# Kernel tuning notes

Measured on AMD Instinct MI355X. Metric: run time of the kernel, lower is better.

## Reference

```python
import jax, jax.numpy as jnp
import numpy as np

B, N = 512, 4
OBS, OBSU, ID = 128, 64, 16
STATE = OBS + OBSU - ID  # 176
M1, M2, G1, A = 256, 256, 256, 16
E = 128  # hypernet_embed


def setup_inputs() -> dict:
    key = jax.random.key(0)
    ks = jax.random.split(key, 24)

    def W(k, shape):
        return jax.random.normal(k, shape, dtype=jnp.float32) * 0.05

    inp = {"input": jax.random.normal(ks[0], (B, N, OBS + OBSU), dtype=jnp.float32)}
    # layer1_hypernet: Linear(ID, 10*E)
    inp["l1_W"] = W(ks[1], (10 * E, ID)); inp["l1_b"] = W(ks[2], (10 * E,))
    # hyper_net{i}_w / hyper_net{i}_b : Linear(E, in*out) / Linear(E, out)
    inp["w1W"] = W(ks[3], (STATE * M1, E)); inp["w1b"] = W(ks[4], (STATE * M1,))
    inp["b1W"] = W(ks[5], (M1, E));        inp["b1b"] = W(ks[6], (M1,))
    inp["w2W"] = W(ks[7], (M1 * M2, E));   inp["w2b"] = W(ks[8], (M1 * M2,))
    inp["b2W"] = W(ks[9], (M2, E));        inp["b2b"] = W(ks[10], (M2,))
    inp["w3W"] = W(ks[11], (M2 * M2, E));  inp["w3b"] = W(ks[12], (M2 * M2,))
    inp["b3W"] = W(ks[13], (M2, E));       inp["b3b"] = W(ks[14], (M2,))
    inp["w4W"] = W(ks[15], (M2 * G1, E));  inp["w4b"] = W(ks[16], (M2 * G1,))
    inp["b4W"] = W(ks[17], (G1, E));       inp["b4b"] = W(ks[18], (G1,))
    inp["w5W"] = W(ks[19], (G1 * A, E));   inp["w5b"] = W(ks[20], (G1 * A,))
    inp["b5W"] = W(ks[21], (A, E));        inp["b5b"] = W(ks[22], (A,))
    return inp


def reference(input, l1_W, l1_b, w1W, w1b, b1W, b1b, w2W, w2b, b2W, b2b,
              w3W, w3b, b3W, b3b, w4W, w4b, b4W, b4b, w5W, w5b, b5W, b5b):
    b, n, d = input.shape
    BN = b * n
    ids = input[..., -ID:].reshape(BN, ID)
    x = input[..., :-ID].reshape(BN, d - ID)  # [BN, STATE]
    # layer1_hypernet: ReLU(Linear(ID -> 10E))
    h = jax.nn.relu(ids @ l1_W.T + l1_b)  # [BN, 10E]
    chunk = lambda i: h[:, i * E:(i + 1) * E]

    def layer(x, iw, ib, wW, wb, bW, bb, out_dim, act):
        # generate per-sample weight [BN, in, out] and bias [BN, out]
        Wm = (chunk(iw) @ wW.T + wb).reshape(BN, x.shape[-1], out_dim)
        bm = chunk(ib) @ bW.T + bb
        y = jnp.einsum('bs,bsm->bm', x, Wm) + bm  # batched GEMV
        return jax.nn.relu(y) if act else y

    out = layer(x,   0, 1, w1W, w1b, b1W, b1b, M1, True)
    out = layer(out, 2, 3, w2W, w2b, b2W, b2b, M2, True)
    out = layer(out, 4, 5, w3W, w3b, b3W, b3b, M2, True)
    out = layer(out, 6, 7, w4W, w4b, b4W, b4b, G1, False)  # no ReLU after layer 4
    out = layer(out, 8, 9, w5W, w5b, b5W, b5b, A, True)
    return out.reshape(b, n, A)
```

## Files before the change

### kernel.cpp

```cpp
#include <hip/hip_runtime.h>
#include <hip/hip_bf16.h>

#define E_ 128
#define NSAMP 2048

typedef __attribute__((ext_vector_type(8))) short short8;
typedef __attribute__((ext_vector_type(4))) float floatx4;

__device__ __forceinline__ ushort f2b(float f) {
    union { __hip_bfloat16 h; ushort u; } cv;
    cv.h = __float2bfloat16(f);
    return cv.u;
}

__device__ __forceinline__ void gload_lds16(const ushort* g, ushort* l) {
    __builtin_amdgcn_global_load_lds(
        (const __attribute__((address_space(1))) void*)g,
        (__attribute__((address_space(3))) void*)l, 16, 0, 0);
}

__global__ void hyper_h(const float* __restrict__ input, const float* __restrict__ l1W,
                        const float* __restrict__ l1b, float* __restrict__ h)
{
    int b = blockIdx.x / 5;
    int o = (blockIdx.x % 5) * 256 + threadIdx.x;
    const float* ids = input + (size_t)b * 192 + 176;
    const float* w = l1W + (size_t)o * 16;
    float a = l1b[o];
#pragma unroll
    for (int i = 0; i < 16; i += 4) {
        float4 wv = *(const float4*)(w + i);
        a += ids[i] * wv.x + ids[i + 1] * wv.y + ids[i + 2] * wv.z + ids[i + 3] * wv.w;
    }
    h[(size_t)b * 1280 + o] = fmaxf(a, 0.f);
}

__global__ void x0_t(const float* __restrict__ input, float* __restrict__ xT0)
{
    int idx = blockIdx.x * 256 + threadIdx.x;
    int s = idx >> 11, b = idx & 2047;
    xT0[idx] = input[(size_t)b * 192 + s];
}

__global__ void cvt_layer(const float* __restrict__ wW, const float* __restrict__ wb,
                          const float* __restrict__ bW, ushort* __restrict__ dst,
                          int S, int M)
{
    int i = (blockIdx.x * 256 + threadIdx.x) * 8;
    const int nW = S * M * E_;
    union { ushort o[8]; uint4 v; } u;
    if (i < nW) {
        float4 a = *(const float4*)(wW + i);
        float4 b = *(const float4*)(wW + i + 4);
        u.o[0] = f2b(a.x); u.o[1] = f2b(a.y); u.o[2] = f2b(a.z); u.o[3] = f2b(a.w);
        u.o[4] = f2b(b.x); u.o[5] = f2b(b.y); u.o[6] = f2b(b.z); u.o[7] = f2b(b.w);
    } else {
        int rem = i - nW;
        int slice = rem / (M * E_);
        int r2 = rem - slice * (M * E_);
        int m = r2 >> 7, e = r2 & 127;
        if (slice == 0) {
            const float* src = bW + (size_t)m * E_ + e;
            float4 a = *(const float4*)(src);
            float4 b = *(const float4*)(src + 4);
            u.o[0] = f2b(a.x); u.o[1] = f2b(a.y); u.o[2] = f2b(a.z); u.o[3] = f2b(a.w);
            u.o[4] = f2b(b.x); u.o[5] = f2b(b.y); u.o[6] = f2b(b.z); u.o[7] = f2b(b.w);
        } else {
#pragma unroll
            for (int jj = 0; jj < 8; ++jj) {
                int s = (slice - 1) * 128 + e + jj;
                u.o[jj] = (s < S) ? f2b(wb[(size_t)s * M + m]) : (ushort)0;
            }
        }
    }
    *(uint4*)(dst + i) = u.v;
}

struct P5 { const float* wW[5]; const float* wb[5]; const float* bW[5]; };

__global__ void prep(P5 p, ushort* __restrict__ dst,
                     const float* __restrict__ input, const float* __restrict__ l1W,
                     const float* __restrict__ l1b, float* __restrict__ h,
                     float* __restrict__ xT0)
{
    const int blk = blockIdx.x;
    if (blk < 15555) {
        const size_t offE[6] = {0, 5865472, 14352384, 22839296, 31326208, 31856640};
        const int Sl[5] = {176, 256, 256, 256, 256};
        const int Ml[5] = {256, 256, 256, 256, 16};
        size_t i = ((size_t)blk * 256 + threadIdx.x) * 8;
        if (i >= 31856640) return;
        int l = 0;
#pragma unroll
        for (int k = 1; k < 5; ++k) if (i >= offE[k]) l = k;
        const int S = Sl[l], M = Ml[l];
        const float* wW = p.wW[l];
        const float* wb = p.wb[l];
        const float* bW = p.bW[l];
        int r = (int)(i - offE[l]);
        const int nW = S * M * E_;
        union { ushort o[8]; uint4 v; } u;
        if (r < nW) {
            float4 a = *(const float4*)(wW + r);
            float4 b = *(const float4*)(wW + r + 4);
            u.o[0] = f2b(a.x); u.o[1] = f2b(a.y); u.o[2] = f2b(a.z); u.o[3] = f2b(a.w);
            u.o[4] = f2b(b.x); u.o[5] = f2b(b.y); u.o[6] = f2b(b.z); u.o[7] = f2b(b.w);
        } else {
            int rem = r - nW;
            int slice = rem / (M * E_);
            int r2 = rem - slice * (M * E_);
            int m = r2 >> 7, e = r2 & 127;
            if (slice == 0) {
                const float* src = bW + (size_t)m * E_ + e;
                float4 a = *(const float4*)(src);
                float4 b = *(const float4*)(src + 4);
                u.o[0] = f2b(a.x); u.o[1] = f2b(a.y); u.o[2] = f2b(a.z); u.o[3] = f2b(a.w);
                u.o[4] = f2b(b.x); u.o[5] = f2b(b.y); u.o[6] = f2b(b.z); u.o[7] = f2b(b.w);
            } else {
#pragma unroll
                for (int jj = 0; jj < 8; ++jj) {
                    int s = (slice - 1) * 128 + e + jj;
                    u.o[jj] = (s < S) ? f2b(wb[(size_t)s * M + m]) : (ushort)0;
                }
            }
        }
        *(uint4*)(dst + i) = u.v;
    } else if (blk < 15555 + 10240) {
        const int b2 = blk - 15555;
        const int b = b2 / 5;
        const int o = (b2 % 5) * 256 + threadIdx.x;
        const float* ids = input + (size_t)b * 192 + 176;
        const float* w = l1W + (size_t)o * 16;
        float a = l1b[o];
#pragma unroll
        for (int i = 0; i < 16; i += 4) {
            float4 wv = *(const float4*)(w + i);
            a += ids[i] * wv.x + ids[i + 1] * wv.y + ids[i + 2] * wv.z + ids[i + 3] * wv.w;
        }
        h[(size_t)b * 1280 + o] = fmaxf(a, 0.f);
    } else {
        const int idx = (blk - 25795) * 256 + threadIdx.x;
        const int s = idx >> 11, b = idx & 2047;
        xT0[idx] = input[(size_t)b * 192 + s];
    }
}

__global__ __launch_bounds__(256, 2) void gemm_big(
    const ushort* __restrict__ wWb, const float* __restrict__ h,
    const float* __restrict__ xT, float* __restrict__ partial,
    int S, int iw, int ksplit, int btiles, int ntiles)
{
    __shared__ __align__(16) ushort Bs[2][2 * 128 * 64];
    __shared__ __align__(16) float xs[17 * 128];

    const int tid = threadIdx.x;
    const int bid = blockIdx.x;
    const int xcd = bid & 7;
    const int jj_ = bid >> 3;
    const int combo = xcd + 8 * (jj_ / btiles);
    const int bt = jj_ % btiles;
    const int nt = combo % ntiles;
    const int ks = combo / ntiles;
    const int b0 = bt * 128;
    const int m0 = nt * 128;
    const int total_s = S + 3;
    const int base = total_s / ksplit;
    const int rem = total_s - base * ksplit;
    const int s0 = ks * base + min(ks, rem);
    const int s1v = s0 + base + (ks < rem ? 1 : 0);
    const int sE = min(s1v, S);
    const int ns = sE - s0;

    const int lane = tid & 63;
    const int wave = tid >> 6;
    const int quad = lane >> 4;
    const int lr = lane & 15;
    const int wm0 = wave * 32;

    const int brow = lane >> 3;
    const int bgg = (lane & 7) ^ brow;

    float hreg[2][2][2][8];
#pragma unroll
    for (int i = 0; i < 2; ++i)
#pragma unroll
        for (int p = 0; p < 2; ++p)
#pragma unroll
            for (int k2 = 0; k2 < 2; ++k2) {
                const float* src = h + (size_t)(b0 + wm0 + i * 16 + lr) * 1280
                                     + (size_t)iw * E_ + p * 64 + k2 * 32 + quad * 8;
                float4 v0 = *(const float4*)(src);
                float4 v1 = *(const float4*)(src + 4);
                hreg[i][p][k2][0] = v0.x; hreg[i][p][k2][1] = v0.y;
                hreg[i][p][k2][2] = v0.z; hreg[i][p][k2][3] = v0.w;
                hreg[i][p][k2][4] = v1.x; hreg[i][p][k2][5] = v1.y;
                hreg[i][p][k2][6] = v1.z; hreg[i][p][k2][7] = v1.w;
            }

    for (int idx = tid; idx < ns * 128; idx += 256) {
        int j = idx >> 7, bb2 = idx & 127;
        xs[idx] = xT[(size_t)(s0 + j) * NSAMP + b0 + bb2];
    }

    floatx4 acc[2][8];
#pragma unroll
    for (int i = 0; i < 2; ++i)
#pragma unroll
        for (int j = 0; j < 8; ++j)
            acc[i][j] = (floatx4){0.f, 0.f, 0.f, 0.f};

    auto dmaB = [&](int s, ushort* buf) {
#pragma unroll
        for (int p = 0; p < 2; ++p)
#pragma unroll
            for (int t4 = 0; t4 < 4; ++t4) {
                int rloc = wave * 32 + t4 * 8;
                const ushort* gp = wWb + ((size_t)s * 256 + m0 + rloc + brow) * E_ + p * 64 + bgg * 8;
                gload_lds16(gp, buf + (size_t)p * 8192 + (size_t)rloc * 64 + lane * 8);
            }
    };
    auto dmaBh = [&](int s, int p, ushort* buf) {
#pragma unroll
        for (int t4 = 0; t4 < 4; ++t4) {
            int rloc = wave * 32 + t4 * 8;
            const ushort* gp = wWb + ((size_t)s * 256 + m0 + rloc + brow) * E_ + p * 64 + bgg * 8;
            gload_lds16(gp, buf + (size_t)rloc * 64 + lane * 8);
        }
    };

    __builtin_amdgcn_sched_barrier(0);
    __syncthreads();
    __builtin_amdgcn_sched_barrier(0);
    dmaB(s0, &Bs[0][0]);
    if (ns > 1) dmaB(s0 + 1, &Bs[1][0]);

    for (int si = 0; si < ns; ++si) {
        const float xr0 = xs[si * 128 + wm0 + lr];
        const float xr1 = xs[si * 128 + wm0 + 16 + lr];
        short8 af0[2][2], af1[2][2];
#pragma unroll
        for (int p = 0; p < 2; ++p)
#pragma unroll
            for (int k2 = 0; k2 < 2; ++k2)
#pragma unroll
                for (int j = 0; j < 8; ++j) {
                    af0[p][k2][j] = (short)f2b(xr0 * hreg[0][p][k2][j]);
                    af1[p][k2][j] = (short)f2b(xr1 * hreg[1][p][k2][j]);
                }

        if (si + 1 < ns) asm volatile("s_waitcnt vmcnt(8)" ::: "memory");
        else             asm volatile("s_waitcnt vmcnt(0)" ::: "memory");
        __builtin_amdgcn_sched_barrier(0);
        __builtin_amdgcn_s_barrier();
        __builtin_amdgcn_sched_barrier(0);

        const ushort* bcur = &Bs[si & 1][0];
        __builtin_amdgcn_s_setprio(1);
#pragma unroll
        for (int kk = 0; kk < 4; ++kk) {
            const int p = kk >> 1, k2 = kk & 1;
            const int swz = ((k2 * 4 + quad) ^ (lr & 7)) * 8;
            short8 bfr[8];
#pragma unroll
            for (int j = 0; j < 8; ++j)
                bfr[j] = *(const short8*)&bcur[(size_t)p * 8192 + (size_t)(j * 16 + lr) * 64 + swz];
            const short8 a0 = (p == 0) ? ((k2 == 0) ? af0[0][0] : af0[0][1])
                                       : ((k2 == 0) ? af0[1][0] : af0[1][1]);
            const short8 a1 = (p == 0) ? ((k2 == 0) ? af1[0][0] : af1[0][1])
                                       : ((k2 == 0) ? af1[1][0] : af1[1][1]);
#pragma unroll
            for (int j = 0; j < 8; ++j) {
                acc[0][j] = __builtin_amdgcn_mfma_f32_16x16x32_bf16(a0, bfr[j], acc[0][j], 0, 0, 0);
                acc[1][j] = __builtin_amdgcn_mfma_f32_16x16x32_bf16(a1, bfr[j], acc[1][j], 0, 0, 0);
            }
        }
        __builtin_amdgcn_s_setprio(0);
        __builtin_amdgcn_sched_barrier(0);
        __builtin_amdgcn_s_barrier();
        __builtin_amdgcn_sched_barrier(0);

        if (si + 2 < ns) dmaB(s0 + si + 2, &Bs[si & 1][0]);
    }

    for (int s = sE; s < s1v; ++s) {
        for (int p = 0; p < 2; ++p) {
            __syncthreads();
            dmaBh(s, p, &Bs[0][0]);
            short8 af[2][2];
            if (s == S) {
#pragma unroll
                for (int k2 = 0; k2 < 2; ++k2)
#pragma unroll
                    for (int i = 0; i < 2; ++i) {
                        const float* src = h + (size_t)(b0 + wm0 + i * 16 + lr) * 1280
                                             + (size_t)(iw + 1) * E_ + p * 64 + k2 * 32 + quad * 8;
                        float4 v0 = *(const float4*)(src);
                        float4 v1 = *(const float4*)(src + 4);
                        af[k2][i][0] = (short)f2b(v0.x); af[k2][i][1] = (short)f2b(v0.y);
                        af[k2][i][2] = (short)f2b(v0.z); af[k2][i][3] = (short)f2b(v0.w);
                        af[k2][i][4] = (short)f2b(v1.x); af[k2][i][5] = (short)f2b(v1.y);
                        af[k2][i][6] = (short)f2b(v1.z); af[k2][i][7] = (short)f2b(v1.w);
                    }
            } else {
                const int jbase = (s - S - 1) * 128 + p * 64;
#pragma unroll
                for (int k2 = 0; k2 < 2; ++k2)
#pragma unroll
                    for (int i = 0; i < 2; ++i) {
                        const int b = b0 + wm0 + i * 16 + lr;
#pragma unroll
                        for (int jj = 0; jj < 8; ++jj) {
                            const int sp = jbase + k2 * 32 + quad * 8 + jj;
                            af[k2][i][jj] = (sp < S) ? (short)f2b(xT[(size_t)sp * NSAMP + b]) : (short)0;
                        }
                    }
            }
            __syncthreads();
#pragma unroll
            for (int k2 = 0; k2 < 2; ++k2) {
                const int swz = ((k2 * 4 + quad) ^ (lr & 7)) * 8;
                short8 bfr[8];
#pragma unroll
                for (int j = 0; j < 8; ++j)
                    bfr[j] = *(const short8*)&Bs[0][(size_t)(j * 16 + lr) * 64 + swz];
#pragma unroll
                for (int j = 0; j < 8; ++j) {
                    acc[0][j] = __builtin_amdgcn_mfma_f32_16x16x32_bf16(af[k2][0], bfr[j], acc[0][j], 0, 0, 0);
                    acc[1][j] = __builtin_amdgcn_mfma_f32_16x16x32_bf16(af[k2][1], bfr[j], acc[1][j], 0, 0, 0);
                }
            }
        }
    }

    float* dst = partial + (size_t)ks * NSAMP * 256;
#pragma unroll
    for (int i = 0; i < 2; ++i)
#pragma unroll
        for (int j = 0; j < 8; ++j)
#pragma unroll
            for (int r = 0; r < 4; ++r) {
                const int row = wm0 + i * 16 + quad * 4 + r;
                const int col = j * 16 + lr;
                dst[(size_t)(b0 + row) * 256 + m0 + col] = acc[i][j][r];
            }
}

template<int BM, int BN, int WROWS, int WCOLS>
__global__ __launch_bounds__(256, 2) void gemm_k(
    const ushort* __restrict__ wWb, const float* __restrict__ h,
    const float* __restrict__ xT, float* __restrict__ partial,
    int S, int M, int iw, int ksplit, int btiles, int ntiles)
{
    constexpr int SM = BM / WROWS / 16;
    constexpr int SN = BN / WCOLS / 16;
    constexpr int ASLOTS = BM * 8 / 256;
    constexpr int LDA = 72;

    __shared__ ushort As[BM][LDA];
    __shared__ ushort Bs[BN][LDA];

    const int tid = threadIdx.x;
    const int bt = blockIdx.x % btiles;
    const int nt = (blockIdx.x / btiles) % ntiles;
    const int ks = blockIdx.x / (btiles * ntiles);
    const int b0 = bt * BM;
    const int m0 = nt * BN;
    const int total_s = S + 3;
    const int base = total_s / ksplit;
    const int rem = total_s - base * ksplit;
    const int s0 = ks * base + min(ks, rem);
    const int s1 = s0 + base + (ks < rem ? 1 : 0);

    const int lane = tid & 63;
    const int wave = tid >> 6;
    const int quad = lane >> 4;
    const int lr = lane & 15;
    const int wm0 = (wave / WCOLS) * (BM / WROWS);
    const int wn0 = (wave % WCOLS) * (BN / WCOLS);

    const int tb = tid >> 3;
    const int teg = tid & 7;

    float hreg[ASLOTS][2][8];
#pragma unroll
    for (int k2 = 0; k2 < ASLOTS; ++k2) {
        int b = tb + 32 * k2;
#pragma unroll
        for (int p = 0; p < 2; ++p) {
            const float* src = h + (size_t)(b0 + b) * 1280 + (size_t)iw * E_ + p * 64 + teg * 8;
            float4 v0 = *(const float4*)(src);
            float4 v1 = *(const float4*)(src + 4);
            hreg[k2][p][0] = v0.x; hreg[k2][p][1] = v0.y; hreg[k2][p][2] = v0.z; hreg[k2][p][3] = v0.w;
            hreg[k2][p][4] = v1.x; hreg[k2][p][5] = v1.y; hreg[k2][p][6] = v1.z; hreg[k2][p][7] = v1.w;
        }
    }

    floatx4 acc[SM][SN];
#pragma unroll
    for (int i = 0; i < SM; ++i)
#pragma unroll
        for (int j = 0; j < SN; ++j)
            acc[i][j] = (floatx4){0.f, 0.f, 0.f, 0.f};

    for (int s = s0; s < s1; ++s) {
        float xv[ASLOTS];
        if (s < S) {
#pragma unroll
            for (int k2 = 0; k2 < ASLOTS; ++k2)
                xv[k2] = xT[(size_t)s * NSAMP + b0 + tb + 32 * k2];
        }

#pragma unroll
        for (int p = 0; p < 2; ++p) {
            if (s < S) {
#pragma unroll
                for (int k2 = 0; k2 < ASLOTS; ++k2) {
                    union { ushort o[8]; uint4 v; } u;
#pragma unroll
                    for (int j = 0; j < 8; ++j) u.o[j] = f2b(xv[k2] * hreg[k2][p][j]);
                    *(uint4*)&As[tb + 32 * k2][teg * 8] = u.v;
                }
            } else if (s == S) {
#pragma unroll
                for (int k2 = 0; k2 < ASLOTS; ++k2) {
                    const float* src = h + (size_t)(b0 + tb + 32 * k2) * 1280
                                         + (size_t)(iw + 1) * E_ + p * 64 + teg * 8;
                    float4 v0 = *(const float4*)(src);
                    float4 v1 = *(const float4*)(src + 4);
                    union { ushort o[8]; uint4 v; } u;
                    u.o[0] = f2b(v0.x); u.o[1] = f2b(v0.y); u.o[2] = f2b(v0.z); u.o[3] = f2b(v0.w);
                    u.o[4] = f2b(v1.x); u.o[5] = f2b(v1.y); u.o[6] = f2b(v1.z); u.o[7] = f2b(v1.w);
                    *(uint4*)&As[tb + 32 * k2][teg * 8] = u.v;
                }
            } else {
                int j0 = (s - S - 1) * 128 + p * 64 + teg * 8;
#pragma unroll
                for (int k2 = 0; k2 < ASLOTS; ++k2) {
                    int b = b0 + tb + 32 * k2;
                    union { ushort o[8]; uint4 v; } u;
#pragma unroll
                    for (int jj = 0; jj < 8; ++jj) {
                        int sp = j0 + jj;
                        u.o[jj] = (sp < S) ? f2b(xT[(size_t)sp * NSAMP + b]) : (ushort)0;
                    }
                    *(uint4*)&As[tb + 32 * k2][teg * 8] = u.v;
                }
            }
#pragma unroll
            for (int slot = tid; slot < BN * 8; slot += 256) {
                int m = slot >> 3, eg2 = slot & 7;
                *(uint4*)&Bs[m][eg2 * 8] =
                    *(const uint4*)(wWb + ((size_t)s * M + m0 + m) * E_ + p * 64 + eg2 * 8);
            }
            __syncthreads();
#pragma unroll
            for (int kk = 0; kk < 2; ++kk) {
                short8 af[SM], bfr[SN];
#pragma unroll
                for (int i = 0; i < SM; ++i)
                    af[i] = *(const short8*)&As[wm0 + i * 16 + lr][kk * 32 + quad * 8];
#pragma unroll
                for (int j = 0; j < SN; ++j)
                    bfr[j] = *(const short8*)&Bs[wn0 + j * 16 + lr][kk * 32 + quad * 8];
#pragma unroll
                for (int i = 0; i < SM; ++i)
#pragma unroll
                    for (int j = 0; j < SN; ++j)
                        acc[i][j] = __builtin_amdgcn_mfma_f32_16x16x32_bf16(af[i], bfr[j], acc[i][j], 0, 0, 0);
            }
            __syncthreads();
        }
    }

    float* dst = partial + (size_t)ks * NSAMP * M;
#pragma unroll
    for (int i = 0; i < SM; ++i)
#pragma unroll
        for (int j = 0; j < SN; ++j)
#pragma unroll
            for (int r = 0; r < 4; ++r) {
                int row = wm0 + i * 16 + quad * 4 + r;
                int col = wn0 + j * 16 + lr;
                dst[(size_t)(b0 + row) * M + m0 + col] = acc[i][j][r];
            }
}

__global__ void reduce_mid(const float* __restrict__ partial, const float* __restrict__ bb,
                           float* __restrict__ xTn, int KS, int relu)
{
    __shared__ float t[32][33];
    const int b0 = (blockIdx.x >> 3) * 32;
    const int m0 = (blockIdx.x & 7) * 32;
    const int mo = threadIdx.x & 31;
    const int bs0 = threadIdx.x >> 5;
    const float bv = bb[m0 + mo];
#pragma unroll
    for (int r = 0; r < 4; ++r) {
        const int bs = bs0 + 8 * r;
        const size_t off = (size_t)(b0 + bs) * 256 + m0 + mo;
        float a0 = 0.f, a1 = 0.f, a2 = 0.f, a3 = 0.f;
#pragma unroll
        for (int k = 0; k < 16; k += 4) {
            a0 += partial[(size_t)(k + 0) * (NSAMP * 256) + off];
            a1 += partial[(size_t)(k + 1) * (NSAMP * 256) + off];
            a2 += partial[(size_t)(k + 2) * (NSAMP * 256) + off];
            a3 += partial[(size_t)(k + 3) * (NSAMP * 256) + off];
        }
        float a = (a0 + a1) + (a2 + a3) + bv;
        if (relu) a = fmaxf(a, 0.f);
        t[bs][mo] = a;
    }
    __syncthreads();
    const int bo = threadIdx.x & 31;
    const int ms0 = threadIdx.x >> 5;
#pragma unroll
    for (int r = 0; r < 4; ++r) {
        const int ms = ms0 + 8 * r;
        xTn[(size_t)(m0 + ms) * NSAMP + b0 + bo] = t[bo][ms];
    }
}

__global__ void reduce_out(const float* __restrict__ partial, const float* __restrict__ bb,
                           float* __restrict__ out, int KS)
{
    int idx = blockIdx.x * 256 + threadIdx.x;
    float a0 = 0.f, a1 = 0.f, a2 = 0.f, a3 = 0.f;
#pragma unroll
    for (int k = 0; k < 64; k += 4) {
        a0 += partial[(size_t)(k + 0) * (NSAMP * 16) + idx];
        a1 += partial[(size_t)(k + 1) * (NSAMP * 16) + idx];
        a2 += partial[(size_t)(k + 2) * (NSAMP * 16) + idx];
        a3 += partial[(size_t)(k + 3) * (NSAMP * 16) + idx];
    }
    out[idx] = fmaxf((a0 + a1) + (a2 + a3) + bb[idx & 15], 0.f);
}

extern "C" void kernel_launch(void* const* d_in, const int* in_sizes, int n_in,
                              void* d_out, int out_size, void* d_ws, size_t ws_size,
                              hipStream_t stream)
{
    const float* input = (const float*)d_in[0];
    const float* l1W   = (const float*)d_in[1];
    const float* l1b   = (const float*)d_in[2];

    char* ws = (char*)d_ws;
    const int S_[5] = {176, 256, 256, 256, 256};
    const int M_[5] = {256, 256, 256, 256, 16};
    const size_t offE[6] = {0, 5865472, 14352384, 22839296, 31326208, 31856640};

    const bool fused = ws_size >= (size_t)111947776;

    ushort* wWb5;
    float *h, *xT0, *xT1, *part;
    if (fused) {
        wWb5 = (ushort*)(ws + 0);
        h    = (float*)(ws + 63713280);
        xT0  = (float*)(ws + 74199040);
        xT1  = (float*)(ws + 76296192);
        part = (float*)(ws + 78393344);
    } else {
        wWb5 = (ushort*)(ws + 0);
        h    = (float*)(ws + 16975872);
        xT0  = (float*)(ws + 27461632);
        xT1  = (float*)(ws + 29558784);
        part = (float*)(ws + 31655936);
    }

    if (fused) {
        P5 p;
        for (int i = 0; i < 5; ++i) {
            p.wW[i] = (const float*)d_in[3 + 4 * i];
            p.wb[i] = (const float*)d_in[4 + 4 * i];
            p.bW[i] = (const float*)d_in[5 + 4 * i];
        }
        hipLaunchKernelGGL(prep, dim3(27203), dim3(256), 0, stream,
                           p, wWb5, input, l1W, l1b, h, xT0);
    } else {
        hipLaunchKernelGGL(hyper_h, dim3(2048 * 5), dim3(256), 0, stream, input, l1W, l1b, h);
        hipLaunchKernelGGL(x0_t, dim3(176 * 2048 / 256), dim3(256), 0, stream, input, xT0);
    }

    float* xt[2] = {xT0, xT1};

    for (int i = 0; i < 5; ++i) {
        const float* wW = (const float*)d_in[3 + 4 * i];
        const float* wb = (const float*)d_in[4 + 4 * i];
        const float* bW = (const float*)d_in[5 + 4 * i];
        const float* bb = (const float*)d_in[6 + 4 * i];
        float* xin = xt[i & 1];

        ushort* wWbL;
        if (fused) {
            wWbL = wWb5 + offE[i];
        } else {
            wWbL = wWb5;
            int ntot = (S_[i] + 3) * M_[i] * E_;
            hipLaunchKernelGGL(cvt_layer, dim3(ntot / 2048), dim3(256), 0, stream,
                               wW, wb, bW, wWbL, S_[i], M_[i]);
        }

        if (M_[i] == 256) {
            const int btiles = 16, ntiles = 2, ksplit = 16;
            hipLaunchKernelGGL(gemm_big, dim3(btiles * ntiles * ksplit), dim3(256), 0, stream,
                               wWbL, h, xin, part, S_[i], 2 * i, ksplit, btiles, ntiles);
            hipLaunchKernelGGL(reduce_mid, dim3(512), dim3(256), 0, stream,
                               part, bb, xt[(i + 1) & 1], ksplit, (i < 3) ? 1 : 0);
        } else {
            const int btiles = 8, ntiles = 1, ksplit = 64;
            hipLaunchKernelGGL((gemm_k<256, 16, 4, 1>), dim3(btiles * ntiles * ksplit), dim3(256), 0, stream,
                               wWbL, h, xin, part, S_[i], 16, 2 * i, ksplit, btiles, ntiles);
            hipLaunchKernelGGL(reduce_out, dim3(128), dim3(256), 0, stream,
                               part, bb, (float*)d_out, ksplit);
        }
    }
}
```

Baseline: 500.2 us.

## Fuse split-K partial reduction and bias-ReLU into next layer's GEMM operand load

```diff
diff --git a/kernel.cpp b/kernel.cpp
--- a/kernel.cpp
+++ b/kernel.cpp
@@ -145,9 +145,11 @@
     }
 }
 
+template<int FUSED>
 __global__ __launch_bounds__(256, 2) void gemm_big(
     const ushort* __restrict__ wWb, const float* __restrict__ h,
-    const float* __restrict__ xT, float* __restrict__ partial,
+    const float* __restrict__ xsrc, const float* __restrict__ bbp,
+    float* __restrict__ partial,
     int S, int iw, int ksplit, int btiles, int ntiles)
 {
     __shared__ __align__(16) ushort Bs[2][2 * 128 * 64];
@@ -197,9 +199,34 @@
                 hreg[i][p][k2][6] = v1.z; hreg[i][p][k2][7] = v1.w;
             }
 
-    for (int idx = tid; idx < ns * 128; idx += 256) {
-        int j = idx >> 7, bb2 = idx & 127;
-        xs[idx] = xT[(size_t)(s0 + j) * NSAMP + b0 + bb2];
+    if constexpr (FUSED) {
+        const int sc = tid & 15;
+        const int br = tid >> 4;
+        for (int j0 = 0; j0 < ns; j0 += 16) {
+            const int j = j0 + sc;
+            if (j < ns) {
+                const float bv = bbp[s0 + j];
+#pragma unroll
+                for (int c = 0; c < 8; ++c) {
+                    const int b2 = c * 16 + br;
+                    const float* rp = xsrc + (size_t)(b0 + b2) * 256 + (s0 + j);
+                    float a0 = bv, a1 = 0.f, a2 = 0.f, a3 = 0.f;
+#pragma unroll
+                    for (int k = 0; k < 16; k += 4) {
+                        a0 += rp[(size_t)(k + 0) * (NSAMP * 256)];
+                        a1 += rp[(size_t)(k + 1) * (NSAMP * 256)];
+                        a2 += rp[(size_t)(k + 2) * (NSAMP * 256)];
+                        a3 += rp[(size_t)(k + 3) * (NSAMP * 256)];
+                    }
+                    xs[j * 128 + b2] = fmaxf((a0 + a1) + (a2 + a3), 0.f);
+                }
+            }
+        }
+    } else {
+        for (int idx = tid; idx < ns * 128; idx += 256) {
+            int j = idx >> 7, bb2 = idx & 127;
+            xs[idx] = xsrc[(size_t)(s0 + j) * NSAMP + b0 + bb2];
+        }
     }
 
     floatx4 acc[2][8];
@@ -301,6 +328,38 @@
                         af[k2][i][4] = (short)f2b(v1.x); af[k2][i][5] = (short)f2b(v1.y);
                         af[k2][i][6] = (short)f2b(v1.z); af[k2][i][7] = (short)f2b(v1.w);
                     }
+            } else if constexpr (FUSED) {
+                const int jbase = (s - S - 1) * 128 + p * 64;
+#pragma unroll
+                for (int k2 = 0; k2 < 2; ++k2)
+#pragma unroll
+                    for (int i = 0; i < 2; ++i) {
+                        const int b = b0 + wm0 + i * 16 + lr;
+                        const int spb = jbase + k2 * 32 + quad * 8;
+                        if (spb < S) {
+                            const float* rp = xsrc + (size_t)b * 256 + spb;
+                            float4 A0 = *(const float4*)(bbp + spb);
+                            float4 A1 = *(const float4*)(bbp + spb + 4);
+#pragma unroll 4
+                            for (int k = 0; k < 16; ++k) {
+                                float4 v0 = *(const float4*)(rp + (size_t)k * (NSAMP * 256));
+                                float4 v1 = *(const float4*)(rp + (size_t)k * (NSAMP * 256) + 4);
+                                A0.x += v0.x; A0.y += v0.y; A0.z += v0.z; A0.w += v0.w;
+                                A1.x += v1.x; A1.y += v1.y; A1.z += v1.z; A1.w += v1.w;
+                            }
+                            af[k2][i][0] = (short)f2b(fmaxf(A0.x, 0.f));
+                            af[k2][i][1] = (short)f2b(fmaxf(A0.y, 0.f));
+                            af[k2][i][2] = (short)f2b(fmaxf(A0.z, 0.f));
+                            af[k2][i][3] = (short)f2b(fmaxf(A0.w, 0.f));
+                            af[k2][i][4] = (short)f2b(fmaxf(A1.x, 0.f));
+                            af[k2][i][5] = (short)f2b(fmaxf(A1.y, 0.f));
+                            af[k2][i][6] = (short)f2b(fmaxf(A1.z, 0.f));
+                            af[k2][i][7] = (short)f2b(fmaxf(A1.w, 0.f));
+                        } else {
+#pragma unroll
+                            for (int jj = 0; jj < 8; ++jj) af[k2][i][jj] = (short)0;
+                        }
+                    }
             } else {
                 const int jbase = (s - S - 1) * 128 + p * 64;
 #pragma unroll
@@ -311,7 +370,7 @@
 #pragma unroll
                         for (int jj = 0; jj < 8; ++jj) {
                             const int sp = jbase + k2 * 32 + quad * 8 + jj;
-                            af[k2][i][jj] = (sp < S) ? (short)f2b(xT[(size_t)sp * NSAMP + b]) : (short)0;
+                            af[k2][i][jj] = (sp < S) ? (short)f2b(xsrc[(size_t)sp * NSAMP + b]) : (short)0;
                         }
                     }
             }
@@ -548,25 +607,31 @@
     const int M_[5] = {256, 256, 256, 256, 16};
     const size_t offE[6] = {0, 5865472, 14352384, 22839296, 31326208, 31856640};
 
-    const bool fused = ws_size >= (size_t)111947776;
+    const bool fusedW   = ws_size >= (size_t)111947776;
+    const bool fullfuse = ws_size >= (size_t)145502208;
 
     ushort* wWb5;
-    float *h, *xT0, *xT1, *part;
-    if (fused) {
-        wWb5 = (ushort*)(ws + 0);
-        h    = (float*)(ws + 63713280);
-        xT0  = (float*)(ws + 74199040);
-        xT1  = (float*)(ws + 76296192);
-        part = (float*)(ws + 78393344);
+    float *h, *xT0, *xT1, *part, *part1;
+    if (fusedW) {
+        wWb5  = (ushort*)(ws + 0);
+        h     = (float*)(ws + 63713280);
+        xT0   = (float*)(ws + 74199040);
+        xT1   = (float*)(ws + 76296192);
+        part  = (float*)(ws + 78393344);
+        part1 = (float*)(ws + 111947776);
     } else {
         wWb5 = (ushort*)(ws + 0);
         h    = (float*)(ws + 16975872);
         xT0  = (float*)(ws + 27461632);
         xT1  = (float*)(ws + 29558784);
         part = (float*)(ws + 31655936);
-    }
-
-    if (fused) {
+        part1 = nullptr;
+    }
+
+    const float* bb_[5];
+    for (int i = 0; i < 5; ++i) bb_[i] = (const float*)d_in[6 + 4 * i];
+
+    if (fusedW) {
         P5 p;
         for (int i = 0; i < 5; ++i) {
             p.wW[i] = (const float*)d_in[3 + 4 * i];
@@ -580,17 +645,35 @@
         hipLaunchKernelGGL(x0_t, dim3(176 * 2048 / 256), dim3(256), 0, stream, input, xT0);
     }
 
+    if (fullfuse) {
+        const int btiles = 16, ntiles = 2, ksplit = 16;
+        hipLaunchKernelGGL((gemm_big<0>), dim3(512), dim3(256), 0, stream,
+                           wWb5 + offE[0], h, xT0, nullptr, part, S_[0], 0, ksplit, btiles, ntiles);
+        hipLaunchKernelGGL((gemm_big<1>), dim3(512), dim3(256), 0, stream,
+                           wWb5 + offE[1], h, part, bb_[0], part1, S_[1], 2, ksplit, btiles, ntiles);
+        hipLaunchKernelGGL((gemm_big<1>), dim3(512), dim3(256), 0, stream,
+                           wWb5 + offE[2], h, part1, bb_[1], part, S_[2], 4, ksplit, btiles, ntiles);
+        hipLaunchKernelGGL((gemm_big<1>), dim3(512), dim3(256), 0, stream,
+                           wWb5 + offE[3], h, part, bb_[2], part1, S_[3], 6, ksplit, btiles, ntiles);
+        hipLaunchKernelGGL(reduce_mid, dim3(512), dim3(256), 0, stream,
+                           part1, bb_[3], xT0, 16, 0);
+        hipLaunchKernelGGL((gemm_k<256, 16, 4, 1>), dim3(512), dim3(256), 0, stream,
+                           wWb5 + offE[4], h, xT0, part, S_[4], 16, 8, 64, 8, 1);
+        hipLaunchKernelGGL(reduce_out, dim3(128), dim3(256), 0, stream,
+                           part, bb_[4], (float*)d_out, 64);
+        return;
+    }
+
     float* xt[2] = {xT0, xT1};
-
     for (int i = 0; i < 5; ++i) {
         const float* wW = (const float*)d_in[3 + 4 * i];
         const float* wb = (const float*)d_in[4 + 4 * i];
         const float* bW = (const float*)d_in[5 + 4 * i];
-        const float* bb = (const float*)d_in[6 + 4 * i];
+        const float* bb = bb_[i];
         float* xin = xt[i & 1];
 
         ushort* wWbL;
-        if (fused) {
+        if (fusedW) {
             wWbL = wWb5 + offE[i];
         } else {
             wWbL = wWb5;
@@ -601,16 +684,15 @@
 
         if (M_[i] == 256) {
             const int btiles = 16, ntiles = 2, ksplit = 16;
-            hipLaunchKernelGGL(gemm_big, dim3(btiles * ntiles * ksplit), dim3(256), 0, stream,
-                               wWbL, h, xin, part, S_[i], 2 * i, ksplit, btiles, ntiles);
+            hipLaunchKernelGGL((gemm_big<0>), dim3(btiles * ntiles * ksplit), dim3(256), 0, stream,
+                               wWbL, h, xin, nullptr, part, S_[i], 2 * i, ksplit, btiles, ntiles);
             hipLaunchKernelGGL(reduce_mid, dim3(512), dim3(256), 0, stream,
-                               part, bb, xt[(i + 1) & 1], ksplit, (i < 3) ? 1 : 0);
+                               part, bb, xt[(i + 1) & 1], 16, (i < 3) ? 1 : 0);
         } else {
-            const int btiles = 8, ntiles = 1, ksplit = 64;
-            hipLaunchKernelGGL((gemm_k<256, 16, 4, 1>), dim3(btiles * ntiles * ksplit), dim3(256), 0, stream,
-                               wWbL, h, xin, part, S_[i], 16, 2 * i, ksplit, btiles, ntiles);
+            hipLaunchKernelGGL((gemm_k<256, 16, 4, 1>), dim3(512), dim3(256), 0, stream,
+                               wWbL, h, xin, part, S_[i], 16, 2 * i, 64, 8, 1);
             hipLaunchKernelGGL(reduce_out, dim3(128), dim3(256), 0, stream,
-                               part, bb, (float*)d_out, ksplit);
-        }
-    }
-}
+                               part, bb, (float*)d_out, 64);
+        }
+    }
+}
```

Measured after the change: 668.4 us. +33.6%, slower.
